# Optimization experiments

Hardware: AMD Instinct MI355X
Metric: run time of the kernel (lower is better)

The kernel has to match this reference:

```python
import jax, jax.numpy as jnp
import numpy as np

H = 16
BN_EPS = 1e-12

def setup_inputs() -> dict:
    key = jax.random.key(0)
    ks = jax.random.split(key, 12)
    B, S, D = 2, 2048, 1024
    sc_in = 1.0 / np.sqrt(D)
    inp = {
        "hidden_states": jax.random.normal(ks[0], (B, S, D), jnp.float32),
        "attention_mask": jnp.zeros((B, 1, 1, S), jnp.float32),
        "Wq": jax.random.normal(ks[1], (D, D), jnp.float32) * sc_in,
        "bq": jnp.zeros((D,), jnp.float32),
        "Wk": jax.random.normal(ks[2], (D, D), jnp.float32) * sc_in,
        "bk": jnp.zeros((D,), jnp.float32),
        "Wv": jax.random.normal(ks[3], (D, D), jnp.float32) * sc_in,
        "bv": jnp.zeros((D,), jnp.float32),
        "pW1": jax.random.normal(ks[4], (D, 64), jnp.float32) * sc_in,
        "pb1": jnp.zeros((64,), jnp.float32),
        "bn_gamma": jnp.ones((64,), jnp.float32),
        "bn_beta": jnp.zeros((64,), jnp.float32),
        "bn_mean": jnp.zeros((64,), jnp.float32),
        "bn_var": jnp.ones((64,), jnp.float32),
        "pW2": jax.random.normal(ks[5], (64, H), jnp.float32) * (1.0 / 8.0),
        "pb2": jnp.zeros((H,), jnp.float32),
    }
    return inp


def reference(hidden_states, attention_mask, Wq, bq, Wk, bk, Wv, bv,
              pW1, pb1, bn_gamma, bn_beta, bn_mean, bn_var, pW2, pb2):
    B, S, D = hidden_states.shape
    hd = D // H
    scale = 1.0 / jnp.sqrt(jnp.asarray(hd, hidden_states.dtype))

    def split_heads(x):  # [B,S,D] -> [B,H,S,hd]
        return x.reshape(B, S, H, hd).transpose(0, 2, 1, 3)

    q = split_heads(hidden_states @ Wq + bq)
    k = split_heads(hidden_states @ Wk + bk)
    v = split_heads(hidden_states @ Wv + bv)

    scores = jnp.einsum("bhqd,bhkd->bhqk", q, k) * scale + attention_mask
    probs = jax.nn.softmax(scores, axis=-1)

    # head-gate predictor (layer_id == 0 -> mean pooling over sequence)
    pooled = jnp.mean(hidden_states, axis=1)  # [B,D]
    h = pooled @ pW1 + pb1
    h = (h - bn_mean) * jax.lax.rsqrt(bn_var + BN_EPS) * bn_gamma + bn_beta
    h = jax.nn.relu(h)
    logits = h @ pW2 + pb2  # [B,H]
    # inference-mode gumbel gate: hard threshold at 0
    head_gate = (logits >= 0).astype(probs.dtype)  # [B,H]

    probs = probs * head_gate[:, :, None, None]
    ctx = jnp.einsum("bhqk,bhkd->bhqd", probs, v)
    return ctx.transpose(0, 2, 1, 3).reshape(B, S, D)
```

## Files before the change

kernel.cpp:

```cpp
#include <hip/hip_runtime.h>

#define S_LEN 2048
#define D_DIM 1024
#define NH 16
#define HD 64
#define BATCH 2

#define QK_SCALE 0.18033688011112042f
#define LOG2E 1.4426950408889634f

using s16x8 = __attribute__((ext_vector_type(8))) short;
using u16x8 = __attribute__((ext_vector_type(8))) unsigned short;
using f32x4 = __attribute__((ext_vector_type(4))) float;
using bf16x8v = __attribute__((ext_vector_type(8))) __bf16;

typedef const __attribute__((address_space(1))) unsigned int* gas_ptr;
typedef __attribute__((address_space(3))) unsigned int* las_ptr;

__device__ __forceinline__ unsigned short f32_to_bf16(float f) {
  unsigned int u = __float_as_uint(f);
  u += 0x7FFFu + ((u >> 16) & 1u);
  return (unsigned short)(u >> 16);
}

__device__ __forceinline__ f32x4 mfma_bf16(s16x8 a, s16x8 b, f32x4 c) {
  return __builtin_amdgcn_mfma_f32_16x16x32_bf16(
      __builtin_bit_cast(bf16x8v, a), __builtin_bit_cast(bf16x8v, b), c, 0, 0, 0);
}

__device__ __forceinline__ float exp2_fast(float x) {
  float r;
  asm("v_exp_f32 %0, %1" : "=v"(r) : "v"(x));
  return r;
}

__device__ __forceinline__ unsigned int cvt_pk_bf16(float a, float b) {
  unsigned int r;
  asm("v_cvt_pk_bf16_f32 %0, %1, %2" : "=v"(r) : "v"(a), "v"(b));
  return r;
}

__global__ __launch_bounds__(256) void pool_cvt(const float* __restrict__ hs,
                                                unsigned short* __restrict__ hsb,
                                                float* __restrict__ partial) {
  int bid = blockIdx.x;
  int b = bid & 1;
  int chunk = (bid >> 1) & 31;
  int dq = bid >> 6;
  int d = dq * 256 + threadIdx.x;
  const float* p = hs + ((size_t)b * S_LEN + chunk * 64) * D_DIM + d;
  unsigned short* o = hsb + ((size_t)b * S_LEN + chunk * 64) * D_DIM + d;
  float s = 0.f;
  for (int i = 0; i < 64; ++i) {
    float v = p[(size_t)i * D_DIM];
    s += v;
    o[(size_t)i * D_DIM] = f32_to_bf16(v);
  }
  partial[(size_t)(b * 32 + chunk) * D_DIM + d] = s;
}

__global__ __launch_bounds__(256) void transpose_w3(
    const float* __restrict__ Wq, const float* __restrict__ Wk,
    const float* __restrict__ Wv, unsigned short* __restrict__ WTq,
    unsigned short* __restrict__ WTk, unsigned short* __restrict__ WTv) {
  __shared__ float tile[32][33];
  int z = blockIdx.z;
  const float* W = (z == 0) ? Wq : (z == 1) ? Wk : Wv;
  unsigned short* WT = (z == 0) ? WTq : (z == 1) ? WTk : WTv;
  float scale = (z == 0) ? QK_SCALE : 1.0f;
  int tx = threadIdx.x & 31;
  int ty = threadIdx.x >> 5;
  int c0 = blockIdx.x * 32;
  int r0 = blockIdx.y * 32;
#pragma unroll
  for (int i = 0; i < 4; ++i)
    tile[ty + i * 8][tx] = W[(r0 + ty + i * 8) * D_DIM + c0 + tx];
  __syncthreads();
#pragma unroll
  for (int i = 0; i < 4; ++i)
    WT[(c0 + ty + i * 8) * D_DIM + r0 + tx] = f32_to_bf16(tile[tx][ty + i * 8] * scale);
}

__global__ __launch_bounds__(512) void gate_kernel(
    const float* __restrict__ partial, const float* __restrict__ pW1,
    const float* __restrict__ pb1, const float* __restrict__ gamma,
    const float* __restrict__ beta, const float* __restrict__ mean,
    const float* __restrict__ var, const float* __restrict__ pW2,
    const float* __restrict__ pb2, float* __restrict__ gate) {
  __shared__ float pooled[2 * D_DIM];
  __shared__ float hsh[2][64];
  int t = threadIdx.x;
  for (int idx = t; idx < 2 * D_DIM; idx += 512) {
    int b = idx >> 10, k = idx & 1023;
    float s = 0.f;
#pragma unroll
    for (int c = 0; c < 32; ++c) s += partial[(size_t)(b * 32 + c) * D_DIM + k];
    pooled[idx] = s * (1.0f / 2048.0f);
  }
  __syncthreads();
  int b = t >> 8, jj = (t >> 2) & 63, quarter = t & 3;
  float acc = 0.f;
  for (int k = quarter * 256; k < quarter * 256 + 256; ++k)
    acc += pooled[b * D_DIM + k] * pW1[k * 64 + jj];
  acc += __shfl_xor(acc, 1, 64);
  acc += __shfl_xor(acc, 2, 64);
  if (quarter == 0) {
    acc += pb1[jj];
    acc = (acc - mean[jj]) * rsqrtf(var[jj] + 1e-12f) * gamma[jj] + beta[jj];
    hsh[b][jj] = fmaxf(acc, 0.f);
  }
  __syncthreads();
  if (t < 32) {
    int bb = t >> 4, hh = t & 15;
    float lg = pb2[hh];
#pragma unroll
    for (int kk = 0; kk < 64; ++kk) lg += hsh[bb][kk] * pW2[kk * NH + hh];
    gate[bb * NH + hh] = (lg >= 0.f) ? 1.f : 0.f;
  }
}

__global__ __launch_bounds__(256) void proj_gemm3(
    const unsigned short* __restrict__ A, const unsigned short* __restrict__ BT,
    const float* __restrict__ bq, const float* __restrict__ bk,
    const float* __restrict__ bv, unsigned short* __restrict__ Qb,
    unsigned short* __restrict__ Kb, unsigned short* __restrict__ Vtb) {
  __shared__ __align__(16) unsigned short As[128 * 64];
  __shared__ __align__(16) unsigned short Bs[128 * 64];
  int idx = blockIdx.x;
  int xcd = idx & 7, j = idx >> 3;
  int xm = xcd * 4 + j / 24;
  int yn = j % 24;
  int m0 = xm * 128, n0 = yn * 128;
  int tid = threadIdx.x, wave = tid >> 6, lane = tid & 63;
  int l15 = lane & 15, lhi = lane >> 4;
  int wm = (wave >> 1) * 64, wn = (wave & 1) * 64;
  f32x4 acc[4][4] = {};

  const unsigned short* asrc[4];
  const unsigned short* bsrc[4];
  int ldst[4];
#pragma unroll
  for (int r4 = 0; r4 < 4; ++r4) {
    int o = tid * 16 + r4 * 4096;
    int row = o >> 7;
    int e = ((o & 127) ^ ((row & 7) << 4)) >> 1;
    asrc[r4] = A + (size_t)(m0 + row) * D_DIM + e;
    bsrc[r4] = BT + (size_t)(n0 + row) * D_DIM + e;
    ldst[r4] = o >> 1;
  }
  int rsw = (l15 & 7) << 4;

  for (int k0 = 0; k0 < D_DIM; k0 += 64) {
#pragma unroll
    for (int r4 = 0; r4 < 4; ++r4) {
      __builtin_amdgcn_global_load_lds((gas_ptr)(asrc[r4] + k0),
                                       (las_ptr)(As + ldst[r4]), 16, 0, 0);
      __builtin_amdgcn_global_load_lds((gas_ptr)(bsrc[r4] + k0),
                                       (las_ptr)(Bs + ldst[r4]), 16, 0, 0);
    }
    __syncthreads();
    __builtin_amdgcn_s_setprio(1);
#pragma unroll
    for (int ks = 0; ks < 2; ++ks) {
      s16x8 af[4], bf[4];
#pragma unroll
      for (int mi = 0; mi < 4; ++mi)
        af[mi] = *(const s16x8*)((const char*)As + (wm + mi * 16 + l15) * 128 +
                                 ((ks * 64 + lhi * 16) ^ rsw));
#pragma unroll
      for (int ni = 0; ni < 4; ++ni)
        bf[ni] = *(const s16x8*)((const char*)Bs + (wn + ni * 16 + l15) * 128 +
                                 ((ks * 64 + lhi * 16) ^ rsw));
#pragma unroll
      for (int mi = 0; mi < 4; ++mi)
#pragma unroll
        for (int ni = 0; ni < 4; ++ni)
          acc[mi][ni] = mfma_bf16(af[mi], bf[ni], acc[mi][ni]);
    }
    __builtin_amdgcn_s_setprio(0);
    __syncthreads();
  }

#pragma unroll
  for (int mi = 0; mi < 4; ++mi)
#pragma unroll
    for (int ni = 0; ni < 4; ++ni) {
      int row0 = m0 + wm + mi * 16 + lhi * 4;
      int col = n0 + wn + ni * 16 + l15;
      int seg = col >> 10, c = col & 1023;
      if (seg == 2) {
        float bvv = bv[c];
        int h = c >> 6, d = c & 63;
        int b = row0 >> 11, s = row0 & 2047;
        ushort4 pk;
        pk.x = f32_to_bf16(acc[mi][ni][0] + bvv);
        pk.y = f32_to_bf16(acc[mi][ni][1] + bvv);
        pk.z = f32_to_bf16(acc[mi][ni][2] + bvv);
        pk.w = f32_to_bf16(acc[mi][ni][3] + bvv);
        *(ushort4*)&Vtb[((size_t)(b * NH + h) * HD + d) * S_LEN + s] = pk;
      } else {
        float bb2 = (seg == 0) ? bq[c] * QK_SCALE : bk[c];
        unsigned short* dst = (seg == 0) ? Qb : Kb;
        int h = c >> 6, d = c & 63;
#pragma unroll
        for (int r = 0; r < 4; ++r) {
          int row = row0 + r;
          int b = row >> 11, s = row & 2047;
          dst[((size_t)(b * NH + h) * S_LEN + s) * HD + d] =
              f32_to_bf16(acc[mi][ni][r] + bb2);
        }
      }
    }
}

__global__ __launch_bounds__(256) void attn_kernel(
    const unsigned short* __restrict__ Q, const unsigned short* __restrict__ K,
    const unsigned short* __restrict__ Vt, const float* __restrict__ mask,
    const float* __restrict__ gate, float* __restrict__ Out) {
  __shared__ __align__(16) unsigned short Ks[2][4096];
  __shared__ __align__(16) unsigned short Vs[2][4096];
  __shared__ __align__(16) unsigned short p_lds[4][1024];

  int idx = blockIdx.x;
  int xcd = idx & 7;
  int slot = idx >> 3;
  int qc = slot & 31;
  int r = (slot >> 5) * 8 + xcd;
  int tid = threadIdx.x;
  int wave = tid >> 6, lane = tid & 63;
  int l15 = lane & 15, lhi = lane >> 4;

  float gv = (lane < 32) ? gate[lane] : 0.f;
  unsigned long long live = __ballot(gv != 0.f);
  int W = __popcll(live);
  bool working = (r < W);
  int want = working ? r : (r - W);
  unsigned long long M = working ? live : (~live & 0xFFFFFFFFull);
  int head = 0, c = 0;
#pragma unroll
  for (int hh = 0; hh < 32; ++hh) {
    if ((M >> hh) & 1) {
      if (c == want) head = hh;
      ++c;
    }
  }
  int b = head >> 4, h = head & 15;
  int q0 = qc * 64 + wave * 16;
  int qrow = q0 + l15;

  if (!working) {
    float4 z = {0.f, 0.f, 0.f, 0.f};
    int row = qc * 64 + (tid >> 2);
    float* op = Out + ((size_t)b * S_LEN + row) * D_DIM + h * HD + (tid & 3) * 16;
#pragma unroll
    for (int dd = 0; dd < 4; ++dd) *(float4*)(op + dd * 4) = z;
    return;
  }

  const unsigned short* Qp = Q + (size_t)head * S_LEN * HD;
  const unsigned short* Kp = K + (size_t)head * S_LEN * HD;
  const unsigned short* Vp = Vt + (size_t)head * HD * S_LEN;
  const float* maskp = mask + (size_t)b * S_LEN;

  int psw = (l15 & 7) << 4;
  int oo0 = wave * 2048 + lane * 16;
  int oo1 = oo0 + 1024;
  int row0 = oo0 >> 7, row1 = oo1 >> 7;
  int e0 = ((oo0 & 127) ^ ((row0 & 7) << 4)) >> 1;
  int e1 = ((oo1 & 127) ^ ((row1 & 7) << 4)) >> 1;
  const unsigned short* kb0 = Kp + row0 * HD + e0;
  const unsigned short* kb1 = Kp + row1 * HD + e1;
  const unsigned short* vb0 = Vp + (size_t)row0 * S_LEN + e0;
  const unsigned short* vb1 = Vp + (size_t)row1 * S_LEN + e1;
  unsigned short* ksb = &Ks[0][0];
  unsigned short* vsb = &Vs[0][0];
  int w0 = (wave * 2048) >> 1;
  int w1 = w0 + 512;

#define STAGE(BUFI, KTV)                                                            \
  {                                                                                 \
    __builtin_amdgcn_global_load_lds((gas_ptr)(kb0 + (size_t)(KTV) * HD),           \
                                     (las_ptr)(ksb + (BUFI) * 4096 + w0), 16, 0, 0);\
    __builtin_amdgcn_global_load_lds((gas_ptr)(kb1 + (size_t)(KTV) * HD),           \
                                     (las_ptr)(ksb + (BUFI) * 4096 + w1), 16, 0, 0);\
    __builtin_amdgcn_global_load_lds((gas_ptr)(vb0 + (KTV)),                        \
                                     (las_ptr)(vsb + (BUFI) * 4096 + w0), 16, 0, 0);\
    __builtin_amdgcn_global_load_lds((gas_ptr)(vb1 + (KTV)),                        \
                                     (las_ptr)(vsb + (BUFI) * 4096 + w1), 16, 0, 0);\
  }

  STAGE(0, 0);
  float4 mvc[4];
#pragma unroll
  for (int nf = 0; nf < 4; ++nf)
    mvc[nf] = *(const float4*)(maskp + nf * 16 + lhi * 4);

  s16x8 q_frag[2];
#pragma unroll
  for (int ks = 0; ks < 2; ++ks)
    q_frag[ks] = *(const s16x8*)(Qp + (size_t)qrow * HD + ks * 32 + lhi * 8);

  int swz0 = (lhi * 16) ^ psw;
  int swz1 = (64 + lhi * 16) ^ psw;
  char* pbase = (char*)p_lds + wave * 2048 + l15 * 128;

  f32x4 o_acc[4] = {};
  float s_run = 0.f;

  __syncthreads();

  for (int kt = 0; kt < S_LEN; kt += 64) {
    int buf = (kt >> 6) & 1;
    int ktn = (kt + 64) & (S_LEN - 1);
    STAGE(buf ^ 1, ktn);
    float4 mvn[4];
#pragma unroll
    for (int nf = 0; nf < 4; ++nf)
      mvn[nf] = *(const float4*)(maskp + ktn + nf * 16 + lhi * 4);

    const char* kc = (const char*)ksb + buf * 8192;
    f32x4 sc[4] = {};
    __builtin_amdgcn_s_setprio(1);
#pragma unroll
    for (int nf = 0; nf < 4; ++nf) {
      int rb = (nf * 16 + l15) * 128;
      s16x8 a0 = *(const s16x8*)(kc + (rb + swz0));
      s16x8 a1 = *(const s16x8*)(kc + (rb + swz1));
      sc[nf] = mfma_bf16(a0, q_frag[0], sc[nf]);
      sc[nf] = mfma_bf16(a1, q_frag[1], sc[nf]);
    }
    __builtin_amdgcn_s_setprio(0);

    float psnf[4];
#pragma unroll
    for (int nf = 0; nf < 4; ++nf) {
#pragma unroll
      for (int rr = 0; rr < 4; ++rr)
        sc[nf][rr] = exp2_fast(fmaf(((const float*)&mvc[nf])[rr], LOG2E, sc[nf][rr]));
      psnf[nf] = (sc[nf][0] + sc[nf][1]) + (sc[nf][2] + sc[nf][3]);
    }
    s_run += (psnf[0] + psnf[1]) + (psnf[2] + psnf[3]);

#pragma unroll
    for (int nf = 0; nf < 4; ++nf) {
      uint2 pk;
      pk.x = cvt_pk_bf16(sc[nf][0], sc[nf][1]);
      pk.y = cvt_pk_bf16(sc[nf][2], sc[nf][3]);
      *(uint2*)(pbase + ((nf * 32 + lhi * 8) ^ psw)) = pk;
    }

    const char* vc = (const char*)vsb + buf * 8192;
    __builtin_amdgcn_s_setprio(1);
#pragma unroll
    for (int ks = 0; ks < 2; ++ks) {
      int sw = ks ? swz1 : swz0;
      s16x8 pf = *(const s16x8*)(pbase + ((ks * 64 + lhi * 16) ^ psw));
#pragma unroll
      for (int df = 0; df < 4; ++df) {
        s16x8 vf = *(const s16x8*)(vc + ((df * 16 + l15) * 128 + sw));
        o_acc[df] = mfma_bf16(vf, pf, o_acc[df]);
      }
    }
    __builtin_amdgcn_s_setprio(0);

    __syncthreads();
#pragma unroll
    for (int nf = 0; nf < 4; ++nf) mvc[nf] = mvn[nf];
  }
#undef STAGE

  float s_tot = s_run;
  s_tot += __shfl_xor(s_tot, 16, 64);
  s_tot += __shfl_xor(s_tot, 32, 64);
  float inv = 1.0f / s_tot;

#pragma unroll
  for (int df = 0; df < 4; ++df) {
    float4 ov;
    ov.x = o_acc[df][0] * inv;
    ov.y = o_acc[df][1] * inv;
    ov.z = o_acc[df][2] * inv;
    ov.w = o_acc[df][3] * inv;
    *(float4*)(Out + ((size_t)b * S_LEN + qrow) * D_DIM + h * HD + df * 16 + lhi * 4) = ov;
  }
}


extern "C" void kernel_launch(void* const* d_in, const int* in_sizes, int n_in,
                              void* d_out, int out_size, void* d_ws, size_t ws_size,
                              hipStream_t stream) {
  (void)in_sizes; (void)n_in; (void)out_size; (void)ws_size;
  const float* hs   = (const float*)d_in[0];
  const float* mask = (const float*)d_in[1];
  const float* Wq   = (const float*)d_in[2];
  const float* bq   = (const float*)d_in[3];
  const float* Wk   = (const float*)d_in[4];
  const float* bk   = (const float*)d_in[5];
  const float* Wv   = (const float*)d_in[6];
  const float* bv   = (const float*)d_in[7];
  const float* pW1  = (const float*)d_in[8];
  const float* pb1  = (const float*)d_in[9];
  const float* gam  = (const float*)d_in[10];
  const float* bet  = (const float*)d_in[11];
  const float* mea  = (const float*)d_in[12];
  const float* var  = (const float*)d_in[13];
  const float* pW2  = (const float*)d_in[14];
  const float* pb2  = (const float*)d_in[15];
  float* out = (float*)d_out;

  const size_t MB = 1u << 20;
  char* ws = (char*)d_ws;
  unsigned short* hsb = (unsigned short*)(ws);
  unsigned short* wTq = (unsigned short*)(ws + 8 * MB);
  unsigned short* wTk = (unsigned short*)(ws + 10 * MB);
  unsigned short* wTv = (unsigned short*)(ws + 12 * MB);
  unsigned short* Qb  = (unsigned short*)(ws + 14 * MB);
  unsigned short* Kb  = (unsigned short*)(ws + 22 * MB);
  unsigned short* Vtb = (unsigned short*)(ws + 30 * MB);
  float* partial = (float*)(ws + 38 * MB);
  float* gateb   = (float*)(ws + 38 * MB + 262144);

  pool_cvt<<<256, 256, 0, stream>>>(hs, hsb, partial);
  transpose_w3<<<dim3(32, 32, 3), 256, 0, stream>>>(Wq, Wk, Wv, wTq, wTk, wTv);
  gate_kernel<<<1, 512, 0, stream>>>(partial, pW1, pb1, gam, bet, mea, var, pW2, pb2, gateb);

  proj_gemm3<<<768, 256, 0, stream>>>(hsb, wTq, bq, bk, bv, Qb, Kb, Vtb);

  attn_kernel<<<1024, 256, 0, stream>>>(Qb, Kb, Vtb, mask, gateb, out);
}
```

Measured before the change: 130.1 us.

## Process two 16-row query tiles per wave in attention with 128-thread blocks

The attention kernel now runs two waves per block instead of four, and each wave handles 32 query rows as two 16-row MFMA tiles. Each K and V fragment read from LDS is reused for both tiles, which halves LDS reads per FLOP. The staging loop issues four K and four V async global-to-LDS loads per thread to cover the same 64-key tile with fewer threads. In exchange, register pressure per wave goes up, and there are fewer waves per block to hide load latency.

```diff
diff --git a/kernel.cpp b/kernel.cpp
--- a/kernel.cpp
+++ b/kernel.cpp
@@ -213,13 +213,13 @@
     }
 }
 
-__global__ __launch_bounds__(256) void attn_kernel(
+__global__ __launch_bounds__(128) void attn_kernel(
     const unsigned short* __restrict__ Q, const unsigned short* __restrict__ K,
     const unsigned short* __restrict__ Vt, const float* __restrict__ mask,
     const float* __restrict__ gate, float* __restrict__ Out) {
   __shared__ __align__(16) unsigned short Ks[2][4096];
   __shared__ __align__(16) unsigned short Vs[2][4096];
-  __shared__ __align__(16) unsigned short p_lds[4][1024];
+  __shared__ __align__(16) unsigned short p_lds[2][2][1024];
 
   int idx = blockIdx.x;
   int xcd = idx & 7;
@@ -245,48 +245,45 @@
     }
   }
   int b = head >> 4, h = head & 15;
-  int q0 = qc * 64 + wave * 16;
-  int qrow = q0 + l15;
 
   if (!working) {
     float4 z = {0.f, 0.f, 0.f, 0.f};
-    int row = qc * 64 + (tid >> 2);
-    float* op = Out + ((size_t)b * S_LEN + row) * D_DIM + h * HD + (tid & 3) * 16;
-#pragma unroll
-    for (int dd = 0; dd < 4; ++dd) *(float4*)(op + dd * 4) = z;
+    int row = qc * 64 + (tid >> 1);
+    float* op = Out + ((size_t)b * S_LEN + row) * D_DIM + h * HD + (tid & 1) * 32;
+#pragma unroll
+    for (int dd = 0; dd < 8; ++dd) *(float4*)(op + dd * 4) = z;
     return;
   }
 
+  int qA = qc * 64 + wave * 32 + l15;
+  int qB = qA + 16;
   const unsigned short* Qp = Q + (size_t)head * S_LEN * HD;
   const unsigned short* Kp = K + (size_t)head * S_LEN * HD;
   const unsigned short* Vp = Vt + (size_t)head * HD * S_LEN;
   const float* maskp = mask + (size_t)b * S_LEN;
 
   int psw = (l15 & 7) << 4;
-  int oo0 = wave * 2048 + lane * 16;
-  int oo1 = oo0 + 1024;
-  int row0 = oo0 >> 7, row1 = oo1 >> 7;
-  int e0 = ((oo0 & 127) ^ ((row0 & 7) << 4)) >> 1;
-  int e1 = ((oo1 & 127) ^ ((row1 & 7) << 4)) >> 1;
-  const unsigned short* kb0 = Kp + row0 * HD + e0;
-  const unsigned short* kb1 = Kp + row1 * HD + e1;
-  const unsigned short* vb0 = Vp + (size_t)row0 * S_LEN + e0;
-  const unsigned short* vb1 = Vp + (size_t)row1 * S_LEN + e1;
-  unsigned short* ksb = &Ks[0][0];
-  unsigned short* vsb = &Vs[0][0];
-  int w0 = (wave * 2048) >> 1;
-  int w1 = w0 + 512;
-
-#define STAGE(BUFI, KTV)                                                            \
-  {                                                                                 \
-    __builtin_amdgcn_global_load_lds((gas_ptr)(kb0 + (size_t)(KTV) * HD),           \
-                                     (las_ptr)(ksb + (BUFI) * 4096 + w0), 16, 0, 0);\
-    __builtin_amdgcn_global_load_lds((gas_ptr)(kb1 + (size_t)(KTV) * HD),           \
-                                     (las_ptr)(ksb + (BUFI) * 4096 + w1), 16, 0, 0);\
-    __builtin_amdgcn_global_load_lds((gas_ptr)(vb0 + (KTV)),                        \
-                                     (las_ptr)(vsb + (BUFI) * 4096 + w0), 16, 0, 0);\
-    __builtin_amdgcn_global_load_lds((gas_ptr)(vb1 + (KTV)),                        \
-                                     (las_ptr)(vsb + (BUFI) * 4096 + w1), 16, 0, 0);\
+  const unsigned short* kb[4];
+  const unsigned short* vb[4];
+  int ldst[4];
+#pragma unroll
+  for (int j = 0; j < 4; ++j) {
+    int o = tid * 16 + j * 2048;
+    int row = o >> 7, col = o & 127;
+    int e = (col ^ ((row & 7) << 4)) >> 1;
+    kb[j] = Kp + row * HD + e;
+    vb[j] = Vp + (size_t)row * S_LEN + e;
+    ldst[j] = o >> 1;
+  }
+
+#define STAGE(BUFI, KTV)                                                           \
+  {                                                                                \
+    _Pragma("unroll") for (int j = 0; j < 4; ++j) {                                \
+      __builtin_amdgcn_global_load_lds((gas_ptr)(kb[j] + (size_t)(KTV)*HD),        \
+                                       (las_ptr)(&Ks[BUFI][ldst[j]]), 16, 0, 0);   \
+      __builtin_amdgcn_global_load_lds((gas_ptr)(vb[j] + (KTV)),                   \
+                                       (las_ptr)(&Vs[BUFI][ldst[j]]), 16, 0, 0);   \
+    }                                                                              \
   }
 
   STAGE(0, 0);
@@ -295,17 +292,20 @@
   for (int nf = 0; nf < 4; ++nf)
     mvc[nf] = *(const float4*)(maskp + nf * 16 + lhi * 4);
 
-  s16x8 q_frag[2];
-#pragma unroll
-  for (int ks = 0; ks < 2; ++ks)
-    q_frag[ks] = *(const s16x8*)(Qp + (size_t)qrow * HD + ks * 32 + lhi * 8);
+  s16x8 qfa[2], qfb[2];
+#pragma unroll
+  for (int ks = 0; ks < 2; ++ks) {
+    qfa[ks] = *(const s16x8*)(Qp + (size_t)qA * HD + ks * 32 + lhi * 8);
+    qfb[ks] = *(const s16x8*)(Qp + (size_t)qB * HD + ks * 32 + lhi * 8);
+  }
 
   int swz0 = (lhi * 16) ^ psw;
   int swz1 = (64 + lhi * 16) ^ psw;
-  char* pbase = (char*)p_lds + wave * 2048 + l15 * 128;
-
-  f32x4 o_acc[4] = {};
-  float s_run = 0.f;
+  char* pbaseA = (char*)p_lds + wave * 4096 + l15 * 128;
+  char* pbaseB = pbaseA + 2048;
+
+  f32x4 oa[4] = {}, ob[4] = {};
+  float sa_run = 0.f, sb_run = 0.f;
 
   __syncthreads();
 
@@ -318,47 +318,61 @@
     for (int nf = 0; nf < 4; ++nf)
       mvn[nf] = *(const float4*)(maskp + ktn + nf * 16 + lhi * 4);
 
-    const char* kc = (const char*)ksb + buf * 8192;
-    f32x4 sc[4] = {};
+    const char* kc = (const char*)&Ks[0][0] + buf * 8192;
+    f32x4 sa[4] = {}, sb[4] = {};
     __builtin_amdgcn_s_setprio(1);
 #pragma unroll
     for (int nf = 0; nf < 4; ++nf) {
       int rb = (nf * 16 + l15) * 128;
       s16x8 a0 = *(const s16x8*)(kc + (rb + swz0));
       s16x8 a1 = *(const s16x8*)(kc + (rb + swz1));
-      sc[nf] = mfma_bf16(a0, q_frag[0], sc[nf]);
-      sc[nf] = mfma_bf16(a1, q_frag[1], sc[nf]);
+      sa[nf] = mfma_bf16(a0, qfa[0], sa[nf]);
+      sa[nf] = mfma_bf16(a1, qfa[1], sa[nf]);
+      sb[nf] = mfma_bf16(a0, qfb[0], sb[nf]);
+      sb[nf] = mfma_bf16(a1, qfb[1], sb[nf]);
     }
     __builtin_amdgcn_s_setprio(0);
 
-    float psnf[4];
+    float psa[4], psb[4];
 #pragma unroll
     for (int nf = 0; nf < 4; ++nf) {
 #pragma unroll
-      for (int rr = 0; rr < 4; ++rr)
-        sc[nf][rr] = exp2_fast(fmaf(((const float*)&mvc[nf])[rr], LOG2E, sc[nf][rr]));
-      psnf[nf] = (sc[nf][0] + sc[nf][1]) + (sc[nf][2] + sc[nf][3]);
-    }
-    s_run += (psnf[0] + psnf[1]) + (psnf[2] + psnf[3]);
+      for (int rr = 0; rr < 4; ++rr) {
+        float m2 = ((const float*)&mvc[nf])[rr] * LOG2E;
+        sa[nf][rr] = exp2_fast(sa[nf][rr] + m2);
+        sb[nf][rr] = exp2_fast(sb[nf][rr] + m2);
+      }
+      psa[nf] = (sa[nf][0] + sa[nf][1]) + (sa[nf][2] + sa[nf][3]);
+      psb[nf] = (sb[nf][0] + sb[nf][1]) + (sb[nf][2] + sb[nf][3]);
+    }
+    sa_run += (psa[0] + psa[1]) + (psa[2] + psa[3]);
+    sb_run += (psb[0] + psb[1]) + (psb[2] + psb[3]);
 
 #pragma unroll
     for (int nf = 0; nf < 4; ++nf) {
-      uint2 pk;
-      pk.x = cvt_pk_bf16(sc[nf][0], sc[nf][1]);
-      pk.y = cvt_pk_bf16(sc[nf][2], sc[nf][3]);
-      *(uint2*)(pbase + ((nf * 32 + lhi * 8) ^ psw)) = pk;
-    }
-
-    const char* vc = (const char*)vsb + buf * 8192;
+      uint2 pka, pkb;
+      pka.x = cvt_pk_bf16(sa[nf][0], sa[nf][1]);
+      pka.y = cvt_pk_bf16(sa[nf][2], sa[nf][3]);
+      pkb.x = cvt_pk_bf16(sb[nf][0], sb[nf][1]);
+      pkb.y = cvt_pk_bf16(sb[nf][2], sb[nf][3]);
+      int off = (nf * 32 + lhi * 8) ^ psw;
+      *(uint2*)(pbaseA + off) = pka;
+      *(uint2*)(pbaseB + off) = pkb;
+    }
+
+    const char* vc = (const char*)&Vs[0][0] + buf * 8192;
     __builtin_amdgcn_s_setprio(1);
 #pragma unroll
     for (int ks = 0; ks < 2; ++ks) {
       int sw = ks ? swz1 : swz0;
-      s16x8 pf = *(const s16x8*)(pbase + ((ks * 64 + lhi * 16) ^ psw));
+      int poff = (ks * 64 + lhi * 16) ^ psw;
+      s16x8 pfa = *(const s16x8*)(pbaseA + poff);
+      s16x8 pfb = *(const s16x8*)(pbaseB + poff);
 #pragma unroll
       for (int df = 0; df < 4; ++df) {
         s16x8 vf = *(const s16x8*)(vc + ((df * 16 + l15) * 128 + sw));
-        o_acc[df] = mfma_bf16(vf, pf, o_acc[df]);
+        oa[df] = mfma_bf16(vf, pfa, oa[df]);
+        ob[df] = mfma_bf16(vf, pfb, ob[df]);
       }
     }
     __builtin_amdgcn_s_setprio(0);
@@ -369,19 +383,23 @@
   }
 #undef STAGE
 
-  float s_tot = s_run;
-  s_tot += __shfl_xor(s_tot, 16, 64);
-  s_tot += __shfl_xor(s_tot, 32, 64);
-  float inv = 1.0f / s_tot;
+  float sa_tot = sa_run, sb_tot = sb_run;
+  sa_tot += __shfl_xor(sa_tot, 16, 64);
+  sa_tot += __shfl_xor(sa_tot, 32, 64);
+  sb_tot += __shfl_xor(sb_tot, 16, 64);
+  sb_tot += __shfl_xor(sb_tot, 32, 64);
+  float inva = 1.0f / sa_tot;
+  float invb = 1.0f / sb_tot;
 
 #pragma unroll
   for (int df = 0; df < 4; ++df) {
-    float4 ov;
-    ov.x = o_acc[df][0] * inv;
-    ov.y = o_acc[df][1] * inv;
-    ov.z = o_acc[df][2] * inv;
-    ov.w = o_acc[df][3] * inv;
-    *(float4*)(Out + ((size_t)b * S_LEN + qrow) * D_DIM + h * HD + df * 16 + lhi * 4) = ov;
+    float4 ova, ovb;
+    ova.x = oa[df][0] * inva; ova.y = oa[df][1] * inva;
+    ova.z = oa[df][2] * inva; ova.w = oa[df][3] * inva;
+    ovb.x = ob[df][0] * invb; ovb.y = ob[df][1] * invb;
+    ovb.z = ob[df][2] * invb; ovb.w = ob[df][3] * invb;
+    *(float4*)(Out + ((size_t)b * S_LEN + qA) * D_DIM + h * HD + df * 16 + lhi * 4) = ova;
+    *(float4*)(Out + ((size_t)b * S_LEN + qB) * D_DIM + h * HD + df * 16 + lhi * 4) = ovb;
   }
 }
 
@@ -426,5 +444,5 @@
 
   proj_gemm3<<<768, 256, 0, stream>>>(hsb, wTq, bq, bk, bv, Qb, Kb, Vtb);
 
-  attn_kernel<<<1024, 256, 0, stream>>>(Qb, Kb, Vtb, mask, gateb, out);
-}
+  attn_kernel<<<1024, 128, 0, stream>>>(Qb, Kb, Vtb, mask, gateb, out);
+}
```

Result: slower. 135.7 us (+4.3%).

## Load K fragments directly to registers and merge transpose with gate kernel

Applied to the files above, without the earlier changes.

The attention kernel no longer stages K tiles through LDS. Each lane now loads its K MFMA fragments straight from global memory into registers, prefetched one tile ahead, which removes the K LDS buffers and the LDS reads. Separately, the weight-transpose and gate kernels are merged into one launch, with the gate computed by an extra block, to save a kernel launch. In exchange, the attention kernel uses more registers, and the direct K loads are scattered per-lane global reads that may be less coalesced.

```diff
diff --git a/kernel.cpp b/kernel.cpp
--- a/kernel.cpp
+++ b/kernel.cpp
@@ -59,63 +59,65 @@
   partial[(size_t)(b * 32 + chunk) * D_DIM + d] = s;
 }
 
-__global__ __launch_bounds__(256) void transpose_w3(
+__global__ __launch_bounds__(256) void prep_wg(
     const float* __restrict__ Wq, const float* __restrict__ Wk,
     const float* __restrict__ Wv, unsigned short* __restrict__ WTq,
-    unsigned short* __restrict__ WTk, unsigned short* __restrict__ WTv) {
-  __shared__ float tile[32][33];
-  int z = blockIdx.z;
-  const float* W = (z == 0) ? Wq : (z == 1) ? Wk : Wv;
-  unsigned short* WT = (z == 0) ? WTq : (z == 1) ? WTk : WTv;
-  float scale = (z == 0) ? QK_SCALE : 1.0f;
-  int tx = threadIdx.x & 31;
-  int ty = threadIdx.x >> 5;
-  int c0 = blockIdx.x * 32;
-  int r0 = blockIdx.y * 32;
-#pragma unroll
-  for (int i = 0; i < 4; ++i)
-    tile[ty + i * 8][tx] = W[(r0 + ty + i * 8) * D_DIM + c0 + tx];
-  __syncthreads();
-#pragma unroll
-  for (int i = 0; i < 4; ++i)
-    WT[(c0 + ty + i * 8) * D_DIM + r0 + tx] = f32_to_bf16(tile[tx][ty + i * 8] * scale);
-}
-
-__global__ __launch_bounds__(512) void gate_kernel(
+    unsigned short* __restrict__ WTk, unsigned short* __restrict__ WTv,
     const float* __restrict__ partial, const float* __restrict__ pW1,
     const float* __restrict__ pb1, const float* __restrict__ gamma,
     const float* __restrict__ beta, const float* __restrict__ mean,
     const float* __restrict__ var, const float* __restrict__ pW2,
     const float* __restrict__ pb2, float* __restrict__ gate) {
-  __shared__ float pooled[2 * D_DIM];
-  __shared__ float hsh[2][64];
+  int bid = blockIdx.x;
   int t = threadIdx.x;
-  for (int idx = t; idx < 2 * D_DIM; idx += 512) {
-    int b = idx >> 10, k = idx & 1023;
-    float s = 0.f;
-#pragma unroll
-    for (int c = 0; c < 32; ++c) s += partial[(size_t)(b * 32 + c) * D_DIM + k];
-    pooled[idx] = s * (1.0f / 2048.0f);
-  }
-  __syncthreads();
-  int b = t >> 8, jj = (t >> 2) & 63, quarter = t & 3;
-  float acc = 0.f;
-  for (int k = quarter * 256; k < quarter * 256 + 256; ++k)
-    acc += pooled[b * D_DIM + k] * pW1[k * 64 + jj];
-  acc += __shfl_xor(acc, 1, 64);
-  acc += __shfl_xor(acc, 2, 64);
-  if (quarter == 0) {
-    acc += pb1[jj];
-    acc = (acc - mean[jj]) * rsqrtf(var[jj] + 1e-12f) * gamma[jj] + beta[jj];
-    hsh[b][jj] = fmaxf(acc, 0.f);
-  }
-  __syncthreads();
-  if (t < 32) {
-    int bb = t >> 4, hh = t & 15;
-    float lg = pb2[hh];
-#pragma unroll
-    for (int kk = 0; kk < 64; ++kk) lg += hsh[bb][kk] * pW2[kk * NH + hh];
-    gate[bb * NH + hh] = (lg >= 0.f) ? 1.f : 0.f;
+  if (bid < 3072) {
+    __shared__ float tile[32][33];
+    int z = bid >> 10;
+    int rem = bid & 1023;
+    const float* W = (z == 0) ? Wq : (z == 1) ? Wk : Wv;
+    unsigned short* WT = (z == 0) ? WTq : (z == 1) ? WTk : WTv;
+    float scale = (z == 0) ? QK_SCALE : 1.0f;
+    int tx = t & 31;
+    int ty = t >> 5;
+    int c0 = (rem & 31) * 32;
+    int r0 = (rem >> 5) * 32;
+#pragma unroll
+    for (int i = 0; i < 4; ++i)
+      tile[ty + i * 8][tx] = W[(r0 + ty + i * 8) * D_DIM + c0 + tx];
+    __syncthreads();
+#pragma unroll
+    for (int i = 0; i < 4; ++i)
+      WT[(c0 + ty + i * 8) * D_DIM + r0 + tx] =
+          f32_to_bf16(tile[tx][ty + i * 8] * scale);
+  } else {
+    __shared__ float pooled[2 * D_DIM];
+    __shared__ float hsh[2][64];
+    for (int idx = t; idx < 2 * D_DIM; idx += 256) {
+      int b = idx >> 10, k = idx & 1023;
+      float s = 0.f;
+#pragma unroll
+      for (int c = 0; c < 32; ++c) s += partial[(size_t)(b * 32 + c) * D_DIM + k];
+      pooled[idx] = s * (1.0f / 2048.0f);
+    }
+    __syncthreads();
+    int b = t >> 7, jj = (t >> 1) & 63, half = t & 1;
+    float acc = 0.f;
+    for (int k = half * 512; k < half * 512 + 512; ++k)
+      acc += pooled[b * D_DIM + k] * pW1[k * 64 + jj];
+    acc += __shfl_xor(acc, 1, 64);
+    if (half == 0) {
+      acc += pb1[jj];
+      acc = (acc - mean[jj]) * rsqrtf(var[jj] + 1e-12f) * gamma[jj] + beta[jj];
+      hsh[b][jj] = fmaxf(acc, 0.f);
+    }
+    __syncthreads();
+    if (t < 32) {
+      int bb = t >> 4, hh = t & 15;
+      float lg = pb2[hh];
+#pragma unroll
+      for (int kk = 0; kk < 64; ++kk) lg += hsh[bb][kk] * pW2[kk * NH + hh];
+      gate[bb * NH + hh] = (lg >= 0.f) ? 1.f : 0.f;
+    }
   }
 }
 
@@ -217,7 +219,6 @@
     const unsigned short* __restrict__ Q, const unsigned short* __restrict__ K,
     const unsigned short* __restrict__ Vt, const float* __restrict__ mask,
     const float* __restrict__ gate, float* __restrict__ Out) {
-  __shared__ __align__(16) unsigned short Ks[2][4096];
   __shared__ __align__(16) unsigned short Vs[2][4096];
   __shared__ __align__(16) unsigned short p_lds[4][1024];
 
@@ -268,28 +269,29 @@
   int row0 = oo0 >> 7, row1 = oo1 >> 7;
   int e0 = ((oo0 & 127) ^ ((row0 & 7) << 4)) >> 1;
   int e1 = ((oo1 & 127) ^ ((row1 & 7) << 4)) >> 1;
-  const unsigned short* kb0 = Kp + row0 * HD + e0;
-  const unsigned short* kb1 = Kp + row1 * HD + e1;
   const unsigned short* vb0 = Vp + (size_t)row0 * S_LEN + e0;
   const unsigned short* vb1 = Vp + (size_t)row1 * S_LEN + e1;
-  unsigned short* ksb = &Ks[0][0];
   unsigned short* vsb = &Vs[0][0];
   int w0 = (wave * 2048) >> 1;
   int w1 = w0 + 512;
 
 #define STAGE(BUFI, KTV)                                                            \
   {                                                                                 \
-    __builtin_amdgcn_global_load_lds((gas_ptr)(kb0 + (size_t)(KTV) * HD),           \
-                                     (las_ptr)(ksb + (BUFI) * 4096 + w0), 16, 0, 0);\
-    __builtin_amdgcn_global_load_lds((gas_ptr)(kb1 + (size_t)(KTV) * HD),           \
-                                     (las_ptr)(ksb + (BUFI) * 4096 + w1), 16, 0, 0);\
     __builtin_amdgcn_global_load_lds((gas_ptr)(vb0 + (KTV)),                        \
                                      (las_ptr)(vsb + (BUFI) * 4096 + w0), 16, 0, 0);\
     __builtin_amdgcn_global_load_lds((gas_ptr)(vb1 + (KTV)),                        \
                                      (las_ptr)(vsb + (BUFI) * 4096 + w1), 16, 0, 0);\
   }
 
+  const unsigned short* kfp = Kp + (size_t)l15 * HD + lhi * 8;
+
   STAGE(0, 0);
+  s16x8 kfc[8];
+#pragma unroll
+  for (int ks = 0; ks < 2; ++ks)
+#pragma unroll
+    for (int nf = 0; nf < 4; ++nf)
+      kfc[ks * 4 + nf] = *(const s16x8*)(kfp + (size_t)(nf * 16) * HD + ks * 32);
   float4 mvc[4];
 #pragma unroll
   for (int nf = 0; nf < 4; ++nf)
@@ -313,21 +315,24 @@
     int buf = (kt >> 6) & 1;
     int ktn = (kt + 64) & (S_LEN - 1);
     STAGE(buf ^ 1, ktn);
+    s16x8 kfn[8];
+#pragma unroll
+    for (int ks = 0; ks < 2; ++ks)
+#pragma unroll
+      for (int nf = 0; nf < 4; ++nf)
+        kfn[ks * 4 + nf] =
+            *(const s16x8*)(kfp + (size_t)(ktn + nf * 16) * HD + ks * 32);
     float4 mvn[4];
 #pragma unroll
     for (int nf = 0; nf < 4; ++nf)
       mvn[nf] = *(const float4*)(maskp + ktn + nf * 16 + lhi * 4);
 
-    const char* kc = (const char*)ksb + buf * 8192;
     f32x4 sc[4] = {};
     __builtin_amdgcn_s_setprio(1);
 #pragma unroll
     for (int nf = 0; nf < 4; ++nf) {
-      int rb = (nf * 16 + l15) * 128;
-      s16x8 a0 = *(const s16x8*)(kc + (rb + swz0));
-      s16x8 a1 = *(const s16x8*)(kc + (rb + swz1));
-      sc[nf] = mfma_bf16(a0, q_frag[0], sc[nf]);
-      sc[nf] = mfma_bf16(a1, q_frag[1], sc[nf]);
+      sc[nf] = mfma_bf16(kfc[nf], q_frag[0], sc[nf]);
+      sc[nf] = mfma_bf16(kfc[4 + nf], q_frag[1], sc[nf]);
     }
     __builtin_amdgcn_s_setprio(0);
 
@@ -364,6 +369,8 @@
     __builtin_amdgcn_s_setprio(0);
 
     __syncthreads();
+#pragma unroll
+    for (int i = 0; i < 8; ++i) kfc[i] = kfn[i];
 #pragma unroll
     for (int nf = 0; nf < 4; ++nf) mvc[nf] = mvn[nf];
   }
@@ -421,8 +428,8 @@
   float* gateb   = (float*)(ws + 38 * MB + 262144);
 
   pool_cvt<<<256, 256, 0, stream>>>(hs, hsb, partial);
-  transpose_w3<<<dim3(32, 32, 3), 256, 0, stream>>>(Wq, Wk, Wv, wTq, wTk, wTv);
-  gate_kernel<<<1, 512, 0, stream>>>(partial, pW1, pb1, gam, bet, mea, var, pW2, pb2, gateb);
+  prep_wg<<<3073, 256, 0, stream>>>(Wq, Wk, Wv, wTq, wTk, wTv, partial, pW1, pb1,
+                                    gam, bet, mea, var, pW2, pb2, gateb);
 
   proj_gemm3<<<768, 256, 0, stream>>>(hsb, wTq, bq, bk, bv, Qb, Kb, Vtb);
 
```

Result: slower. 202.4 us (+55.6%).

## Skip projection tiles for gated-off heads and vectorize pooling conversion

Applied to the files above, without the earlier changes.

The QKV projection GEMM now reads the head gate and exits early for 128-column tiles whose two heads are both gated to zero, since their outputs are never used downstream. Separately, the pool/convert kernel is reorganised to use float4 loads, packed bf16 conversion and smaller 16-row chunks. This yields 128 partial sums per batch, so the gate kernel's reduction loop is longer and the gate buffer offset moves. The skip is valid only if the attention kernel already ignores gated heads.

```diff
diff --git a/kernel.cpp b/kernel.cpp
--- a/kernel.cpp
+++ b/kernel.cpp
@@ -44,19 +44,21 @@
                                                 unsigned short* __restrict__ hsb,
                                                 float* __restrict__ partial) {
   int bid = blockIdx.x;
-  int b = bid & 1;
-  int chunk = (bid >> 1) & 31;
-  int dq = bid >> 6;
-  int d = dq * 256 + threadIdx.x;
-  const float* p = hs + ((size_t)b * S_LEN + chunk * 64) * D_DIM + d;
-  unsigned short* o = hsb + ((size_t)b * S_LEN + chunk * 64) * D_DIM + d;
-  float s = 0.f;
-  for (int i = 0; i < 64; ++i) {
-    float v = p[(size_t)i * D_DIM];
-    s += v;
-    o[(size_t)i * D_DIM] = f32_to_bf16(v);
-  }
-  partial[(size_t)(b * 32 + chunk) * D_DIM + d] = s;
+  int b = bid >> 7;
+  int chunk = bid & 127;
+  int t = threadIdx.x;
+  const float* p = hs + ((size_t)b * S_LEN + chunk * 16) * D_DIM + t * 4;
+  unsigned short* o = hsb + ((size_t)b * S_LEN + chunk * 16) * D_DIM + t * 4;
+  float4 s = {0.f, 0.f, 0.f, 0.f};
+  for (int i = 0; i < 16; ++i) {
+    float4 v = *(const float4*)(p + (size_t)i * D_DIM);
+    s.x += v.x; s.y += v.y; s.z += v.z; s.w += v.w;
+    uint2 pk;
+    pk.x = cvt_pk_bf16(v.x, v.y);
+    pk.y = cvt_pk_bf16(v.z, v.w);
+    *(uint2*)(o + (size_t)i * D_DIM) = pk;
+  }
+  *(float4*)&partial[(size_t)(b * 128 + chunk) * D_DIM + t * 4] = s;
 }
 
 __global__ __launch_bounds__(256) void transpose_w3(
@@ -93,8 +95,7 @@
   for (int idx = t; idx < 2 * D_DIM; idx += 512) {
     int b = idx >> 10, k = idx & 1023;
     float s = 0.f;
-#pragma unroll
-    for (int c = 0; c < 32; ++c) s += partial[(size_t)(b * 32 + c) * D_DIM + k];
+    for (int c = 0; c < 128; ++c) s += partial[(size_t)(b * 128 + c) * D_DIM + k];
     pooled[idx] = s * (1.0f / 2048.0f);
   }
   __syncthreads();
@@ -122,8 +123,9 @@
 __global__ __launch_bounds__(256) void proj_gemm3(
     const unsigned short* __restrict__ A, const unsigned short* __restrict__ BT,
     const float* __restrict__ bq, const float* __restrict__ bk,
-    const float* __restrict__ bv, unsigned short* __restrict__ Qb,
-    unsigned short* __restrict__ Kb, unsigned short* __restrict__ Vtb) {
+    const float* __restrict__ bv, const float* __restrict__ gate,
+    unsigned short* __restrict__ Qb, unsigned short* __restrict__ Kb,
+    unsigned short* __restrict__ Vtb) {
   __shared__ __align__(16) unsigned short As[128 * 64];
   __shared__ __align__(16) unsigned short Bs[128 * 64];
   int idx = blockIdx.x;
@@ -131,6 +133,11 @@
   int xm = xcd * 4 + j / 24;
   int yn = j % 24;
   int m0 = xm * 128, n0 = yn * 128;
+
+  int gb = m0 >> 11;
+  int h0 = (n0 & 1023) >> 6;
+  if (gate[gb * NH + h0] == 0.f && gate[gb * NH + h0 + 1] == 0.f) return;
+
   int tid = threadIdx.x, wave = tid >> 6, lane = tid & 63;
   int l15 = lane & 15, lhi = lane >> 4;
   int wm = (wave >> 1) * 64, wn = (wave & 1) * 64;
@@ -418,13 +425,13 @@
   unsigned short* Kb  = (unsigned short*)(ws + 22 * MB);
   unsigned short* Vtb = (unsigned short*)(ws + 30 * MB);
   float* partial = (float*)(ws + 38 * MB);
-  float* gateb   = (float*)(ws + 38 * MB + 262144);
+  float* gateb   = (float*)(ws + 39 * MB);
 
   pool_cvt<<<256, 256, 0, stream>>>(hs, hsb, partial);
   transpose_w3<<<dim3(32, 32, 3), 256, 0, stream>>>(Wq, Wk, Wv, wTq, wTk, wTv);
   gate_kernel<<<1, 512, 0, stream>>>(partial, pW1, pb1, gam, bet, mea, var, pW2, pb2, gateb);
 
-  proj_gemm3<<<768, 256, 0, stream>>>(hsb, wTq, bq, bk, bv, Qb, Kb, Vtb);
+  proj_gemm3<<<768, 256, 0, stream>>>(hsb, wTq, bq, bk, bv, gateb, Qb, Kb, Vtb);
 
   attn_kernel<<<1024, 256, 0, stream>>>(Qb, Kb, Vtb, mask, gateb, out);
 }
```

Measured after the change: 244.5 us. 88.0% more time.
